# Kernel tuning notes

Hardware: AMD Instinct MI355X
Metric: run time of the kernel (lower is better)

The kernel has to match this reference:

```python
import jax, jax.numpy as jnp
import numpy as np

N, E = 50000, 800000
DN, DE, H = 64, 32, 4
NODE_SCALE = float(np.sqrt(DN))
EDGE_SCALE = float(np.sqrt(DE))


def _linear_init(key, fan_in, fan_out):
    k1, k2 = jax.random.split(key)
    s = 1.0 / np.sqrt(fan_in)
    w = jax.random.uniform(k1, (fan_in, fan_out), minval=-s, maxval=s, dtype=jnp.float32)
    b = jax.random.uniform(k2, (fan_out,), minval=-s, maxval=s, dtype=jnp.float32)
    return w, b


def setup_inputs() -> dict:
    key = jax.random.key(0)
    ks = jax.random.split(key, 12)
    inp = {}
    inp['node_inputs'] = jax.random.normal(ks[0], (N, DN), dtype=jnp.float32)
    inp['edge_inputs'] = jax.random.normal(ks[1], (E, DE), dtype=jnp.float32)
    inp['src'] = jax.random.randint(ks[2], (E,), 0, N, dtype=jnp.int32)
    inp['dst'] = jax.random.randint(ks[3], (E,), 0, N, dtype=jnp.int32)
    # query / key MessageProjection params, value LinearProjection params
    specs = [('qn', DN, H * DN, ks[4]), ('qe', DE, H, ks[5]),
             ('kn', DN, H * DN, ks[6]), ('ke', DE, H, ks[7]),
             ('vn', DN, H * DN, ks[8]), ('ve', DE, H * DE, ks[9])]
    for name, fi, fo, k in specs:
        w, b = _linear_init(k, fi, fo)
        inp[name + '_w'] = w
        inp[name + '_b'] = b
    return inp


def _message_proj(x, e, src, dst, nw, nb, ew, eb):
    # node projection: relu(Linear) -> [N, H, DN]; edge weight: sigmoid(Linear) -> [E, H, 1]
    p = jax.nn.relu(x @ nw + nb).reshape(-1, H, DN)
    w = jax.nn.sigmoid(e @ ew + eb).reshape(-1, H, 1)
    msg = p[src] + w  # u_add_e -> [E, H, DN]
    ssum = jax.ops.segment_sum(msg, dst, num_segments=N)
    deg = jax.ops.segment_sum(jnp.ones((E, 1, 1), msg.dtype), dst, num_segments=N)
    agg = jnp.where(deg > 0, ssum / jnp.maximum(deg, 1.0), 0.0)  # mean reduce, 0 for isolated nodes
    return agg, w


def _attention(q, k, scale):
    # scores over heads: [*, H, H]; exp -> clamp(-5,5) -> softmax (matches torch order)
    s = jnp.clip(jnp.exp(jnp.einsum('nhd,ngd->nhg', q, k) / scale), -5.0, 5.0)
    return jax.nn.softmax(s, axis=-1)


def reference(node_inputs, edge_inputs, src, dst,
              qn_w, qn_b, qe_w, qe_b, kn_w, kn_b, ke_w, ke_b,
              vn_w, vn_b, ve_w, ve_b):
    node_q, edge_q = _message_proj(node_inputs, edge_inputs, src, dst, qn_w, qn_b, qe_w, qe_b)
    node_k, edge_k = _message_proj(node_inputs, edge_inputs, src, dst, kn_w, kn_b, ke_w, ke_b)
    node_v = jax.nn.relu(node_inputs @ vn_w + vn_b).reshape(-1, H, DN)
    edge_v = jax.nn.relu(edge_inputs @ ve_w + ve_b).reshape(-1, H, DE)
    node_attn = _attention(node_q, node_k, NODE_SCALE)  # [N, H, H]
    edge_attn = _attention(edge_q, edge_k, EDGE_SCALE)  # [E, H, H]
    node_emb = jnp.einsum('nhg,ngd->nhd', node_attn, node_v).mean(-2)  # [N, DN]
    edge_emb = jnp.einsum('ehg,egd->ehd', edge_attn, edge_v).mean(-2)  # [E, DE]
    return node_emb, edge_emb
```

## Files before the change

### kernel.cpp

```cpp
#include <hip/hip_runtime.h>
#include <math.h>

#define NN 50000
#define NE 800000

__device__ __forceinline__ unsigned bf16_2(float lo, float hi){
  unsigned a = __float_as_uint(lo), b = __float_as_uint(hi);
  unsigned ra = (a + 0x7fffu + ((a >> 16) & 1u)) >> 16;
  unsigned rb = (b + 0x7fffu + ((b >> 16) & 1u)) >> 16;
  return ra | (rb << 16);
}
__device__ __forceinline__ float bflo(unsigned u){ return __uint_as_float(u << 16); }
__device__ __forceinline__ float bfhi(unsigned u){ return __uint_as_float(u & 0xffff0000u); }

__global__ void k_transpose(const float* __restrict__ s, float* __restrict__ d, int R, int C){
  int idx = blockIdx.x * 256 + threadIdx.x;
  if (idx < R * C){
    int i = idx / C;
    int j = idx - i * C;
    d[j * R + i] = s[idx];
  }
}

__global__ __launch_bounds__(256) void k_node_proj(
    const float* __restrict__ x,
    const float* __restrict__ wtq, const float* __restrict__ bq,
    const float* __restrict__ wtk, const float* __restrict__ bk,
    const float* __restrict__ wtv, const float* __restrict__ bv,
    float* __restrict__ pqk, float* __restrict__ pv){
  int n = blockIdx.x * 256 + threadIdx.x;
  if (n >= NN) return;
  int p = blockIdx.y;
  const float* wt = (p == 0) ? wtq : (p == 1) ? wtk : wtv;
  const float* bb = (p == 0) ? bq  : (p == 1) ? bk  : bv;
  float* out = (p == 0) ? pqk + (size_t)n * 512
             : (p == 1) ? pqk + (size_t)n * 512 + 256
                        : pv  + (size_t)n * 256;
  float xs[64];
  const float4* xv = (const float4*)(x + (size_t)n * 64);
  #pragma unroll
  for (int i = 0; i < 16; i++){
    float4 t = xv[i];
    xs[4*i+0] = t.x; xs[4*i+1] = t.y; xs[4*i+2] = t.z; xs[4*i+3] = t.w;
  }
  for (int j4 = 0; j4 < 64; j4++){
    const float* w0 = wt + (size_t)j4 * 256;
    float a0 = bb[4*j4+0], a1 = bb[4*j4+1], a2 = bb[4*j4+2], a3 = bb[4*j4+3];
    #pragma unroll
    for (int c = 0; c < 64; c++){
      float xc = xs[c];
      a0 = fmaf(xc, w0[c],       a0);
      a1 = fmaf(xc, w0[64 + c],  a1);
      a2 = fmaf(xc, w0[128 + c], a2);
      a3 = fmaf(xc, w0[192 + c], a3);
    }
    float4 o = { fmaxf(a0, 0.f), fmaxf(a1, 0.f), fmaxf(a2, 0.f), fmaxf(a3, 0.f) };
    *(float4*)(out + 4 * j4) = o;
  }
}

__device__ __forceinline__ void attn_mix(const float* dots, float inv_scale, float* cg){
  cg[0] = cg[1] = cg[2] = cg[3] = 0.f;
  #pragma unroll
  for (int h = 0; h < 4; h++){
    float sv[4], mx = -1e30f;
    #pragma unroll
    for (int g = 0; g < 4; g++){
      sv[g] = fminf(expf(dots[h*4 + g] * inv_scale), 5.f);
      mx = fmaxf(mx, sv[g]);
    }
    float rs = 0.f;
    #pragma unroll
    for (int g = 0; g < 4; g++){ sv[g] = expf(sv[g] - mx); rs += sv[g]; }
    float ir = 1.f / rs;
    #pragma unroll
    for (int g = 0; g < 4; g++) cg[g] += sv[g] * ir;
  }
  #pragma unroll
  for (int g = 0; g < 4; g++) cg[g] *= 0.25f;
}

__global__ __launch_bounds__(256) void k_edge_gate(
    const float* __restrict__ einp, const int* __restrict__ dstv,
    const float* __restrict__ qet, const float* __restrict__ qeb,
    const float* __restrict__ ket, const float* __restrict__ keb,
    int* __restrict__ counts, uint4* __restrict__ qwkw){
  int e = blockIdx.x * 256 + threadIdx.x;
  float es[32];
  const float4* ev4 = (const float4*)(einp + (size_t)e * 32);
  #pragma unroll
  for (int i = 0; i < 8; i++){
    float4 t = ev4[i];
    es[4*i+0] = t.x; es[4*i+1] = t.y; es[4*i+2] = t.z; es[4*i+3] = t.w;
  }
  float qw[4], kw[4];
  #pragma unroll
  for (int h = 0; h < 4; h++){
    float aq = qeb[h], ak = keb[h];
    #pragma unroll
    for (int c = 0; c < 32; c++){
      aq = fmaf(es[c], qet[h*32 + c], aq);
      ak = fmaf(es[c], ket[h*32 + c], ak);
    }
    qw[h] = 1.f / (1.f + expf(-aq));
    kw[h] = 1.f / (1.f + expf(-ak));
  }
  atomicAdd(&counts[dstv[e]], 1);
  uint4 o;
  o.x = bf16_2(qw[0], qw[1]);
  o.y = bf16_2(qw[2], qw[3]);
  o.z = bf16_2(kw[0], kw[1]);
  o.w = bf16_2(kw[2], kw[3]);
  qwkw[e] = o;
}

__global__ __launch_bounds__(256) void k_edge_gemm(
    const float* __restrict__ einp, const uint4* __restrict__ qwkw,
    const float* __restrict__ vet, const float* __restrict__ veb,
    float* __restrict__ edge_out){
  __shared__ float es_t[256 * 32];
  __shared__ float cg_t[256 * 4];
  int tid  = threadIdx.x;
  int wid  = tid >> 6;
  int lane = tid & 63;
  size_t blk_e = (size_t)blockIdx.x * 256;

  float w0[32], w1[32];
  {
    const float4* r0 = (const float4*)(vet + lane * 32);
    const float4* r1 = (const float4*)(vet + (lane + 64) * 32);
    #pragma unroll
    for (int i = 0; i < 8; i++){
      float4 a = r0[i], b = r1[i];
      w0[4*i+0]=a.x; w0[4*i+1]=a.y; w0[4*i+2]=a.z; w0[4*i+3]=a.w;
      w1[4*i+0]=b.x; w1[4*i+1]=b.y; w1[4*i+2]=b.z; w1[4*i+3]=b.w;
    }
  }
  float bias0 = veb[lane], bias1 = veb[lane + 64];

  const float4* src4 = (const float4*)(einp + blk_e * 32);
  float4* st4 = (float4*)es_t;
  #pragma unroll
  for (int r = 0; r < 8; r++) st4[r * 256 + tid] = src4[r * 256 + tid];
  {
    uint4 qk = qwkw[blk_e + tid];
    float qw[4] = { bflo(qk.x), bfhi(qk.x), bflo(qk.y), bfhi(qk.y) };
    float kw[4] = { bflo(qk.z), bfhi(qk.z), bflo(qk.w), bfhi(qk.w) };
    const float inv_scale = 0.17677669529663687f;
    float dots[16];
    #pragma unroll
    for (int h = 0; h < 4; h++)
      #pragma unroll
      for (int g = 0; g < 4; g++) dots[h*4 + g] = qw[h] * kw[g];
    float cg[4];
    attn_mix(dots, inv_scale, cg);
    float4 o = { cg[0], cg[1], cg[2], cg[3] };
    *(float4*)(cg_t + tid * 4) = o;
  }
  __syncthreads();

  int g0 = lane >> 5;
  for (int i0 = 0; i0 < 64; i0 += 2){
    int ea = wid * 64 + i0;
    const float4* xa4 = (const float4*)(es_t + ea * 32);
    const float4* xb4 = xa4 + 8;
    float a0 = bias0, a1 = bias1, c0 = bias0, c1 = bias1;
    #pragma unroll
    for (int c4 = 0; c4 < 8; c4++){
      float4 xa = xa4[c4], xb = xb4[c4];
      a0 = fmaf(xa.x, w0[4*c4+0], a0);
      a0 = fmaf(xa.y, w0[4*c4+1], a0);
      a0 = fmaf(xa.z, w0[4*c4+2], a0);
      a0 = fmaf(xa.w, w0[4*c4+3], a0);
      a1 = fmaf(xa.x, w1[4*c4+0], a1);
      a1 = fmaf(xa.y, w1[4*c4+1], a1);
      a1 = fmaf(xa.z, w1[4*c4+2], a1);
      a1 = fmaf(xa.w, w1[4*c4+3], a1);
      c0 = fmaf(xb.x, w0[4*c4+0], c0);
      c0 = fmaf(xb.y, w0[4*c4+1], c0);
      c0 = fmaf(xb.z, w0[4*c4+2], c0);
      c0 = fmaf(xb.w, w0[4*c4+3], c0);
      c1 = fmaf(xb.x, w1[4*c4+0], c1);
      c1 = fmaf(xb.y, w1[4*c4+1], c1);
      c1 = fmaf(xb.z, w1[4*c4+2], c1);
      c1 = fmaf(xb.w, w1[4*c4+3], c1);
    }
    float cga0 = cg_t[ea*4 + g0],       cga2 = cg_t[ea*4 + g0 + 2];
    float cgb0 = cg_t[(ea+1)*4 + g0],   cgb2 = cg_t[(ea+1)*4 + g0 + 2];
    float oa = cga0 * fmaxf(a0, 0.f) + cga2 * fmaxf(a1, 0.f);
    float ob = cgb0 * fmaxf(c0, 0.f) + cgb2 * fmaxf(c1, 0.f);
    oa += __shfl_xor(oa, 32, 64);
    ob += __shfl_xor(ob, 32, 64);
    float val = (lane < 32) ? oa : ob;
    edge_out[(blk_e + (size_t)ea) * 32 + lane] = val;
  }
}

__global__ __launch_bounds__(1024) void k_scan1(const int* __restrict__ counts,
                                                int* __restrict__ offsets,
                                                int* __restrict__ bsums){
  __shared__ int sd[1024];
  int tid = threadIdx.x;
  int gid = blockIdx.x * 1024 + tid;
  int v = (gid < NN) ? counts[gid] : 0;
  sd[tid] = v;
  __syncthreads();
  for (int off = 1; off < 1024; off <<= 1){
    int t = (tid >= off) ? sd[tid - off] : 0;
    __syncthreads();
    sd[tid] += t;
    __syncthreads();
  }
  int incl = sd[tid];
  if (gid < NN) offsets[gid] = incl - v;
  if (tid == 1023) bsums[blockIdx.x] = incl;
}

__global__ void k_scan2(int* __restrict__ bsums, int nb){
  int run = 0;
  for (int i = 0; i < nb; i++){ int t = bsums[i]; bsums[i] = run; run += t; }
}

__global__ __launch_bounds__(1024) void k_scan3(int* __restrict__ offsets,
                                                const int* __restrict__ bsums){
  int gid = blockIdx.x * 1024 + threadIdx.x;
  if (gid < NN) offsets[gid] += bsums[blockIdx.x];
  if (gid == 0) offsets[NN] = NE;
}

__global__ __launch_bounds__(256) void k_fill(const int* __restrict__ dstv,
                                              const int* __restrict__ offsets,
                                              int* __restrict__ cursor,
                                              int* __restrict__ csr){
  int e = blockIdx.x * 256 + threadIdx.x;
  if (e >= NE) return;
  int d = dstv[e];
  int pos = offsets[d] + atomicAdd(&cursor[d], 1);
  csr[pos] = e;
}

__global__ __launch_bounds__(256) void k_node_agg(
    const int* __restrict__ srcv, const int* __restrict__ offsets,
    const int* __restrict__ csr, const uint4* __restrict__ qwkw,
    const float* __restrict__ pqk, const float* __restrict__ pv,
    float* __restrict__ node_out){
  __shared__ float tile[4][512];
  int wid  = threadIdx.x >> 6;
  int lane = threadIdx.x & 63;
  int n = blockIdx.x * 4 + wid;
  int off0 = offsets[n], off1 = offsets[n + 1];
  float4 qa = {0.f,0.f,0.f,0.f}, ka = {0.f,0.f,0.f,0.f};
  float qs0=0.f,qs1=0.f,qs2=0.f,qs3=0.f, ks0=0.f,ks1=0.f,ks2=0.f,ks3=0.f;
  int i = off0;
  int e_cur = 0, s_cur = 0;
  if (i < off1){ e_cur = csr[i]; s_cur = srcv[e_cur]; }
  while (i < off1){
    int e_nxt = 0, s_nxt = 0;
    if (i + 1 < off1){ e_nxt = csr[i + 1]; s_nxt = srcv[e_nxt]; }
    const float4* pr = (const float4*)(pqk + (size_t)s_cur * 512);
    float4 a = pr[lane];
    float4 b = pr[64 + lane];
    uint4 qk = qwkw[e_cur];
    qa.x += a.x; qa.y += a.y; qa.z += a.z; qa.w += a.w;
    ka.x += b.x; ka.y += b.y; ka.z += b.z; ka.w += b.w;
    qs0 += bflo(qk.x); qs1 += bfhi(qk.x); qs2 += bflo(qk.y); qs3 += bfhi(qk.y);
    ks0 += bflo(qk.z); ks1 += bfhi(qk.z); ks2 += bflo(qk.w); ks3 += bfhi(qk.w);
    e_cur = e_nxt; s_cur = s_nxt;
    i++;
  }
  float* tl = tile[wid];
  ((float4*)tl)[lane]      = qa;
  ((float4*)tl)[64 + lane] = ka;
  __syncthreads();
  float qh[4], kh[4];
  int deg = off1 - off0;
  float qsv[4] = { qs0, qs1, qs2, qs3 };
  float ksv[4] = { ks0, ks1, ks2, ks3 };
  if (deg > 0){
    float inv = 1.f / (float)deg;
    #pragma unroll
    for (int h = 0; h < 4; h++){
      qh[h] = (tl[h*64 + lane]       + qsv[h]) * inv;
      kh[h] = (tl[256 + h*64 + lane] + ksv[h]) * inv;
    }
  } else {
    #pragma unroll
    for (int h = 0; h < 4; h++){ qh[h] = 0.f; kh[h] = 0.f; }
  }
  float dots[16];
  #pragma unroll
  for (int h = 0; h < 4; h++)
    #pragma unroll
    for (int g = 0; g < 4; g++) dots[h*4 + g] = qh[h] * kh[g];
  #pragma unroll
  for (int m = 1; m < 64; m <<= 1){
    #pragma unroll
    for (int t = 0; t < 16; t++) dots[t] += __shfl_xor(dots[t], m, 64);
  }
  const float inv_ns = 0.125f;
  float cg[4];
  attn_mix(dots, inv_ns, cg);
  const float* vb = pv + (size_t)n * 256;
  float o = 0.f;
  #pragma unroll
  for (int g = 0; g < 4; g++) o = fmaf(cg[g], vb[g*64 + lane], o);
  node_out[(size_t)n * 64 + lane] = o;
}

extern "C" void kernel_launch(void* const* d_in, const int* in_sizes, int n_in,
                              void* d_out, int out_size, void* d_ws, size_t ws_size,
                              hipStream_t stream) {
  const float* node_inputs = (const float*)d_in[0];
  const float* edge_inputs = (const float*)d_in[1];
  const int*   srcv        = (const int*)d_in[2];
  const int*   dstv        = (const int*)d_in[3];
  const float* qn_w = (const float*)d_in[4];
  const float* qn_b = (const float*)d_in[5];
  const float* qe_w = (const float*)d_in[6];
  const float* qe_b = (const float*)d_in[7];
  const float* kn_w = (const float*)d_in[8];
  const float* kn_b = (const float*)d_in[9];
  const float* ke_w = (const float*)d_in[10];
  const float* ke_b = (const float*)d_in[11];
  const float* vn_w = (const float*)d_in[12];
  const float* vn_b = (const float*)d_in[13];
  const float* ve_w = (const float*)d_in[14];
  const float* ve_b = (const float*)d_in[15];

  float* out      = (float*)d_out;
  float* node_out = out;
  float* edge_out = out + (size_t)NN * 64;

  float* ws = (float*)d_ws;
  float* pqk    = ws;
  float* pv     = pqk + (size_t)NN * 512;
  uint4* qwkw   = (uint4*)(pv + (size_t)NN * 256);
  float* wt_qn  = (float*)(qwkw + NE);
  float* wt_kn  = wt_qn + 16384;
  float* wt_vn  = wt_kn + 16384;
  float* wt_ve  = wt_vn + 16384;
  float* wt_qe  = wt_ve + 4096;
  float* wt_ke  = wt_qe + 128;
  int* counts   = (int*)(wt_ke + 128);
  int* cursor   = counts + NN;
  int* offsets  = cursor + NN;
  int* csr      = offsets + NN + 1;
  int* bsums    = csr + NE;

  hipMemsetAsync(counts, 0, (size_t)2 * NN * sizeof(int), stream);

  k_transpose<<<(16384 + 255) / 256, 256, 0, stream>>>(qn_w, wt_qn, 64, 256);
  k_transpose<<<(16384 + 255) / 256, 256, 0, stream>>>(kn_w, wt_kn, 64, 256);
  k_transpose<<<(16384 + 255) / 256, 256, 0, stream>>>(vn_w, wt_vn, 64, 256);
  k_transpose<<<(4096  + 255) / 256, 256, 0, stream>>>(ve_w, wt_ve, 32, 128);
  k_transpose<<<1, 256, 0, stream>>>(qe_w, wt_qe, 32, 4);
  k_transpose<<<1, 256, 0, stream>>>(ke_w, wt_ke, 32, 4);

  k_edge_gate<<<NE / 256, 256, 0, stream>>>(
      edge_inputs, dstv, wt_qe, qe_b, wt_ke, ke_b, counts, qwkw);
  k_edge_gemm<<<NE / 256, 256, 0, stream>>>(
      edge_inputs, qwkw, wt_ve, ve_b, edge_out);

  k_node_proj<<<dim3((NN + 255) / 256, 3), 256, 0, stream>>>(
      node_inputs, wt_qn, qn_b, wt_kn, kn_b, wt_vn, vn_b, pqk, pv);

  const int SB = (NN + 1023) / 1024;
  k_scan1<<<SB, 1024, 0, stream>>>(counts, offsets, bsums);
  k_scan2<<<1, 1, 0, stream>>>(bsums, SB);
  k_scan3<<<SB, 1024, 0, stream>>>(offsets, bsums);
  k_fill<<<NE / 256, 256, 0, stream>>>(dstv, offsets, cursor, csr);

  k_node_agg<<<NN / 4, 256, 0, stream>>>(
      srcv, offsets, csr, qwkw, pqk, pv, node_out);
}
```

Measured before the change: 871.8 us.

## Store node Q/K projections in bf16, pack src into CSR, merge transposes

Node query/key projections are now written as interleaved bf16 pairs, halving the gather traffic in the node aggregation. The CSR entries store (edge, src) pairs so the aggregation avoids a dependent srcv load, and its loop handles two edges per iteration for more memory-level parallelism. The six weight-transpose launches are merged into one, and the serial block-sum scan becomes a wave-level shuffle scan. The bf16 storage adds rounding error to the aggregated Q/K means.

```diff
diff --git a/kernel.cpp b/kernel.cpp
--- a/kernel.cpp
+++ b/kernel.cpp
@@ -13,8 +13,21 @@
 __device__ __forceinline__ float bflo(unsigned u){ return __uint_as_float(u << 16); }
 __device__ __forceinline__ float bfhi(unsigned u){ return __uint_as_float(u & 0xffff0000u); }
 
-__global__ void k_transpose(const float* __restrict__ s, float* __restrict__ d, int R, int C){
-  int idx = blockIdx.x * 256 + threadIdx.x;
+__global__ __launch_bounds__(256) void k_transpose_all(
+    const float* __restrict__ qnw, const float* __restrict__ knw,
+    const float* __restrict__ vnw, const float* __restrict__ vew,
+    const float* __restrict__ qew, const float* __restrict__ kew,
+    float* __restrict__ wqn, float* __restrict__ wkn, float* __restrict__ wvn,
+    float* __restrict__ wve, float* __restrict__ wqe, float* __restrict__ wke){
+  int b = blockIdx.x;
+  const float* s; float* d; int R, C, base;
+  if (b < 64)       { s = qnw; d = wqn; R = 64; C = 256; base = b; }
+  else if (b < 128) { s = knw; d = wkn; R = 64; C = 256; base = b - 64; }
+  else if (b < 192) { s = vnw; d = wvn; R = 64; C = 256; base = b - 128; }
+  else if (b < 208) { s = vew; d = wve; R = 32; C = 128; base = b - 192; }
+  else if (b == 208){ s = qew; d = wqe; R = 32; C = 4;   base = 0; }
+  else              { s = kew; d = wke; R = 32; C = 4;   base = 0; }
+  int idx = base * 256 + threadIdx.x;
   if (idx < R * C){
     int i = idx / C;
     int j = idx - i * C;
@@ -27,15 +40,12 @@
     const float* __restrict__ wtq, const float* __restrict__ bq,
     const float* __restrict__ wtk, const float* __restrict__ bk,
     const float* __restrict__ wtv, const float* __restrict__ bv,
-    float* __restrict__ pqk, float* __restrict__ pv){
+    unsigned* __restrict__ pqk, float* __restrict__ pv){
   int n = blockIdx.x * 256 + threadIdx.x;
   if (n >= NN) return;
   int p = blockIdx.y;
   const float* wt = (p == 0) ? wtq : (p == 1) ? wtk : wtv;
   const float* bb = (p == 0) ? bq  : (p == 1) ? bk  : bv;
-  float* out = (p == 0) ? pqk + (size_t)n * 512
-             : (p == 1) ? pqk + (size_t)n * 512 + 256
-                        : pv  + (size_t)n * 256;
   float xs[64];
   const float4* xv = (const float4*)(x + (size_t)n * 64);
   #pragma unroll
@@ -54,8 +64,15 @@
       a2 = fmaf(xc, w0[128 + c], a2);
       a3 = fmaf(xc, w0[192 + c], a3);
     }
-    float4 o = { fmaxf(a0, 0.f), fmaxf(a1, 0.f), fmaxf(a2, 0.f), fmaxf(a3, 0.f) };
-    *(float4*)(out + 4 * j4) = o;
+    a0 = fmaxf(a0, 0.f); a1 = fmaxf(a1, 0.f);
+    a2 = fmaxf(a2, 0.f); a3 = fmaxf(a3, 0.f);
+    if (p == 2){
+      float4 o = { a0, a1, a2, a3 };
+      *(float4*)(pv + (size_t)n * 256 + 4 * j4) = o;
+    } else {
+      uint2 o = { bf16_2(a0, a1), bf16_2(a2, a3) };
+      *(uint2*)(pqk + (size_t)n * 256 + j4 * 4 + (p == 1 ? 2 : 0)) = o;
+    }
   }
 }
 
@@ -217,8 +234,15 @@
 }
 
 __global__ void k_scan2(int* __restrict__ bsums, int nb){
-  int run = 0;
-  for (int i = 0; i < nb; i++){ int t = bsums[i]; bsums[i] = run; run += t; }
+  int tid = threadIdx.x;
+  int v = (tid < nb) ? bsums[tid] : 0;
+  for (int off = 1; off < 64; off <<= 1){
+    int t = __shfl_up(v, off, 64);
+    if (tid >= off) v += t;
+  }
+  int ex = __shfl_up(v, 1, 64);
+  if (tid == 0) ex = 0;
+  if (tid < nb) bsums[tid] = ex;
 }
 
 __global__ __launch_bounds__(1024) void k_scan3(int* __restrict__ offsets,
@@ -228,22 +252,22 @@
   if (gid == 0) offsets[NN] = NE;
 }
 
-__global__ __launch_bounds__(256) void k_fill(const int* __restrict__ dstv,
-                                              const int* __restrict__ offsets,
-                                              int* __restrict__ cursor,
-                                              int* __restrict__ csr){
+__global__ __launch_bounds__(256) void k_fill(
+    const int* __restrict__ dstv, const int* __restrict__ srcv,
+    const int* __restrict__ offsets, int* __restrict__ cursor,
+    int2* __restrict__ csr2){
   int e = blockIdx.x * 256 + threadIdx.x;
   if (e >= NE) return;
   int d = dstv[e];
+  int s = srcv[e];
   int pos = offsets[d] + atomicAdd(&cursor[d], 1);
-  csr[pos] = e;
+  csr2[pos] = make_int2(e, s);
 }
 
 __global__ __launch_bounds__(256) void k_node_agg(
-    const int* __restrict__ srcv, const int* __restrict__ offsets,
-    const int* __restrict__ csr, const uint4* __restrict__ qwkw,
-    const float* __restrict__ pqk, const float* __restrict__ pv,
-    float* __restrict__ node_out){
+    const int* __restrict__ offsets, const int2* __restrict__ csr2,
+    const uint4* __restrict__ qwkw, const uint4* __restrict__ pqk,
+    const float* __restrict__ pv, float* __restrict__ node_out){
   __shared__ float tile[4][512];
   int wid  = threadIdx.x >> 6;
   int lane = threadIdx.x & 63;
@@ -252,21 +276,30 @@
   float4 qa = {0.f,0.f,0.f,0.f}, ka = {0.f,0.f,0.f,0.f};
   float qs0=0.f,qs1=0.f,qs2=0.f,qs3=0.f, ks0=0.f,ks1=0.f,ks2=0.f,ks3=0.f;
   int i = off0;
-  int e_cur = 0, s_cur = 0;
-  if (i < off1){ e_cur = csr[i]; s_cur = srcv[e_cur]; }
-  while (i < off1){
-    int e_nxt = 0, s_nxt = 0;
-    if (i + 1 < off1){ e_nxt = csr[i + 1]; s_nxt = srcv[e_nxt]; }
-    const float4* pr = (const float4*)(pqk + (size_t)s_cur * 512);
-    float4 a = pr[lane];
-    float4 b = pr[64 + lane];
-    uint4 qk = qwkw[e_cur];
-    qa.x += a.x; qa.y += a.y; qa.z += a.z; qa.w += a.w;
-    ka.x += b.x; ka.y += b.y; ka.z += b.z; ka.w += b.w;
-    qs0 += bflo(qk.x); qs1 += bfhi(qk.x); qs2 += bflo(qk.y); qs3 += bfhi(qk.y);
-    ks0 += bflo(qk.z); ks1 += bfhi(qk.z); ks2 += bflo(qk.w); ks3 += bfhi(qk.w);
-    e_cur = e_nxt; s_cur = s_nxt;
-    i++;
+  while (i + 2 <= off1){
+    int2 Ea = csr2[i], Eb = csr2[i + 1];
+    uint4 ua = pqk[(size_t)Ea.y * 64 + lane];
+    uint4 ub = pqk[(size_t)Eb.y * 64 + lane];
+    uint4 ga = qwkw[Ea.x];
+    uint4 gb = qwkw[Eb.x];
+    qa.x += bflo(ua.x); qa.y += bfhi(ua.x); qa.z += bflo(ua.y); qa.w += bfhi(ua.y);
+    ka.x += bflo(ua.z); ka.y += bfhi(ua.z); ka.z += bflo(ua.w); ka.w += bfhi(ua.w);
+    qa.x += bflo(ub.x); qa.y += bfhi(ub.x); qa.z += bflo(ub.y); qa.w += bfhi(ub.y);
+    ka.x += bflo(ub.z); ka.y += bfhi(ub.z); ka.z += bflo(ub.w); ka.w += bfhi(ub.w);
+    qs0 += bflo(ga.x) + bflo(gb.x); qs1 += bfhi(ga.x) + bfhi(gb.x);
+    qs2 += bflo(ga.y) + bflo(gb.y); qs3 += bfhi(ga.y) + bfhi(gb.y);
+    ks0 += bflo(ga.z) + bflo(gb.z); ks1 += bfhi(ga.z) + bfhi(gb.z);
+    ks2 += bflo(ga.w) + bflo(gb.w); ks3 += bfhi(ga.w) + bfhi(gb.w);
+    i += 2;
+  }
+  if (i < off1){
+    int2 Ea = csr2[i];
+    uint4 ua = pqk[(size_t)Ea.y * 64 + lane];
+    uint4 ga = qwkw[Ea.x];
+    qa.x += bflo(ua.x); qa.y += bfhi(ua.x); qa.z += bflo(ua.y); qa.w += bfhi(ua.y);
+    ka.x += bflo(ua.z); ka.y += bfhi(ua.z); ka.z += bflo(ua.w); ka.w += bfhi(ua.w);
+    qs0 += bflo(ga.x); qs1 += bfhi(ga.x); qs2 += bflo(ga.y); qs3 += bfhi(ga.y);
+    ks0 += bflo(ga.z); ks1 += bfhi(ga.z); ks2 += bflo(ga.w); ks3 += bfhi(ga.w);
   }
   float* tl = tile[wid];
   ((float4*)tl)[lane]      = qa;
@@ -332,8 +365,8 @@
   float* edge_out = out + (size_t)NN * 64;
 
   float* ws = (float*)d_ws;
-  float* pqk    = ws;
-  float* pv     = pqk + (size_t)NN * 512;
+  unsigned* pqk = (unsigned*)ws;
+  float* pv     = (float*)(pqk + (size_t)NN * 256);
   uint4* qwkw   = (uint4*)(pv + (size_t)NN * 256);
   float* wt_qn  = (float*)(qwkw + NE);
   float* wt_kn  = wt_qn + 16384;
@@ -344,17 +377,14 @@
   int* counts   = (int*)(wt_ke + 128);
   int* cursor   = counts + NN;
   int* offsets  = cursor + NN;
-  int* csr      = offsets + NN + 1;
-  int* bsums    = csr + NE;
+  int2* csr2    = (int2*)(offsets + NN + 2);
+  int* bsums    = (int*)(csr2 + NE);
 
   hipMemsetAsync(counts, 0, (size_t)2 * NN * sizeof(int), stream);
 
-  k_transpose<<<(16384 + 255) / 256, 256, 0, stream>>>(qn_w, wt_qn, 64, 256);
-  k_transpose<<<(16384 + 255) / 256, 256, 0, stream>>>(kn_w, wt_kn, 64, 256);
-  k_transpose<<<(16384 + 255) / 256, 256, 0, stream>>>(vn_w, wt_vn, 64, 256);
-  k_transpose<<<(4096  + 255) / 256, 256, 0, stream>>>(ve_w, wt_ve, 32, 128);
-  k_transpose<<<1, 256, 0, stream>>>(qe_w, wt_qe, 32, 4);
-  k_transpose<<<1, 256, 0, stream>>>(ke_w, wt_ke, 32, 4);
+  k_transpose_all<<<210, 256, 0, stream>>>(
+      qn_w, kn_w, vn_w, ve_w, qe_w, ke_w,
+      wt_qn, wt_kn, wt_vn, wt_ve, wt_qe, wt_ke);
 
   k_edge_gate<<<NE / 256, 256, 0, stream>>>(
       edge_inputs, dstv, wt_qe, qe_b, wt_ke, ke_b, counts, qwkw);
@@ -366,10 +396,10 @@
 
   const int SB = (NN + 1023) / 1024;
   k_scan1<<<SB, 1024, 0, stream>>>(counts, offsets, bsums);
-  k_scan2<<<1, 1, 0, stream>>>(bsums, SB);
+  k_scan2<<<1, 64, 0, stream>>>(bsums, SB);
   k_scan3<<<SB, 1024, 0, stream>>>(offsets, bsums);
-  k_fill<<<NE / 256, 256, 0, stream>>>(dstv, offsets, cursor, csr);
+  k_fill<<<NE / 256, 256, 0, stream>>>(dstv, srcv, offsets, cursor, csr2);
 
   k_node_agg<<<NN / 4, 256, 0, stream>>>(
-      srcv, offsets, csr, qwkw, pqk, pv, node_out);
-}
+      offsets, csr2, qwkw, (const uint4*)pqk, pv, node_out);
+}
```

Result: faster. 771.9 us (-11.5%).
